# Performance work log

Hardware: AMD Instinct MI355X
Metric: run time of the kernel (lower is better)

## Reference

```python
import jax, jax.numpy as jnp
import numpy as np

N_NODES = 100000
N_GRAPHS = 128

def _graph_conv(x, W, b, s, d, n_nodes):
    """DGL GraphConv with norm='both': D_dst^{-1/2} A D_src^{-1/2} X W + b."""
    ones = jnp.ones(s.shape[0], x.dtype)
    deg_out = jax.ops.segment_sum(ones, s, num_segments=n_nodes)  # src out-degree
    deg_in = jax.ops.segment_sum(ones, d, num_segments=n_nodes)   # dst in-degree
    norm_src = jnp.where(deg_out > 0, 1.0 / jnp.sqrt(jnp.maximum(deg_out, 1.0)), 0.0)
    norm_dst = jnp.where(deg_in > 0, 1.0 / jnp.sqrt(jnp.maximum(deg_in, 1.0)), 0.0)
    h = x * norm_src[:, None]                    # [N, F]
    agg = jax.ops.segment_sum(h[s], d, num_segments=n_nodes)  # SpMM gather-scatter
    rst = (agg @ W) * norm_dst[:, None] + b
    return rst

def _hetero_layer(x, Ws, bs, src, dst, n_nodes):
    # HeteroGraphConv aggregate='sum' over relations (fixed small set -> loop ok)
    out = jnp.zeros((n_nodes, Ws.shape[-1]), x.dtype)
    for r in range(Ws.shape[0]):
        out = out + _graph_conv(x, Ws[r], bs[r], src[r], dst[r], n_nodes)
    return out

def setup_inputs() -> dict:
    key = jax.random.key(0)
    ks = jax.random.split(key, 8)
    feat = jax.random.normal(ks[0], (N_NODES, 256), dtype=jnp.float32)
    src = jax.random.randint(ks[1], (3, 400000), 0, N_NODES)
    dst = jax.random.randint(ks[2], (3, 400000), 0, N_NODES)
    graph_ids = jnp.sort(jax.random.randint(ks[3], (N_NODES,), 0, N_GRAPHS))
    W1 = jax.random.normal(ks[4], (3, 256, 256), dtype=jnp.float32) * 0.06
    b1 = jnp.zeros((3, 256), dtype=jnp.float32)
    W2 = jax.random.normal(ks[5], (3, 256, 256), dtype=jnp.float32) * 0.06
    b2 = jnp.zeros((3, 256), dtype=jnp.float32)
    return {"feat": feat, "src": src, "dst": dst, "graph_ids": graph_ids,
            "W1": W1, "b1": b1, "W2": W2, "b2": b2}

def reference(feat, src, dst, graph_ids, W1, b1, W2, b2):
    n_nodes = feat.shape[0]
    h = _hetero_layer(feat, W1, b1, src, dst, n_nodes)
    h = jax.nn.relu(h)
    h = _hetero_layer(h, W2, b2, src, dst, n_nodes)
    # AvgPooling over batched graphs
    sums = jax.ops.segment_sum(h, graph_ids, num_segments=N_GRAPHS)
    counts = jax.ops.segment_sum(jnp.ones(n_nodes, h.dtype), graph_ids, num_segments=N_GRAPHS)
    return sums / jnp.maximum(counts, 1.0)[:, None]
```

## Files before the change

kernel.cpp:

```cpp
#include <hip/hip_runtime.h>
#include <stdint.h>

#define NN 100000
#define NE 400000
#define NR 3
#define NF 256
#define NK 768
#define NG 128
#define SCAN_NB ((NN + 1023) / 1024)

typedef __attribute__((ext_vector_type(4))) unsigned short ushortx4;
typedef __attribute__((ext_vector_type(8))) unsigned short ushortx8;
typedef __attribute__((ext_vector_type(8))) short short8;
typedef __attribute__((ext_vector_type(4))) float floatx4;

static __device__ __forceinline__ unsigned short f2bfu(float f) {
  union { float f; uint32_t u; } c; c.f = f;
  uint32_t x = c.u;
  uint32_t r = (x + 0x7fffu + ((x >> 16) & 1u)) >> 16;
  return (unsigned short)r;
}
static __device__ __forceinline__ float bfu2f(unsigned short u) {
  union { uint32_t u; float f; } c; c.u = ((uint32_t)u) << 16;
  return c.f;
}

static __device__ __forceinline__ void gload16(const void* g, void* l) {
  __builtin_amdgcn_global_load_lds(
      (const __attribute__((address_space(1))) uint32_t*)g,
      (__attribute__((address_space(3))) uint32_t*)l, 16, 0, 0);
}


__global__ __launch_bounds__(256) void degree_kernel(
    const int* __restrict__ src, const int* __restrict__ dst,
    int* __restrict__ deg_out, int* __restrict__ deg_in) {
  int t = blockIdx.x * 256 + threadIdx.x;
  int r = blockIdx.y;
  if (t < NE) {
    atomicAdd(&deg_out[r * NN + src[r * NE + t]], 1);
    atomicAdd(&deg_in[r * NN + dst[r * NE + t]], 1);
  }
}

__global__ __launch_bounds__(128) void gcount_kernel(
    const int* __restrict__ gid, int* __restrict__ gcount) {
  int g = threadIdx.x;
  int lo = 0, hi = NN;
  while (lo < hi) { int mid = (lo + hi) >> 1; if (gid[mid] < g) lo = mid + 1; else hi = mid; }
  int a = lo;
  lo = 0; hi = NN;
  while (lo < hi) { int mid = (lo + hi) >> 1; if (gid[mid] < g + 1) lo = mid + 1; else hi = mid; }
  gcount[g] = lo - a;
}

__global__ __launch_bounds__(256) void norm_kernel(
    const int* __restrict__ deg_out, const int* __restrict__ deg_in,
    float* __restrict__ n_src, float* __restrict__ n_dst) {
  int t = blockIdx.x * 256 + threadIdx.x;
  if (t < NR * NN) {
    int dof = deg_out[t], din = deg_in[t];
    n_src[t] = dof > 0 ? rsqrtf((float)dof) : 0.f;
    n_dst[t] = din > 0 ? rsqrtf((float)din) : 0.f;
  }
}


__global__ __launch_bounds__(256) void scan_phaseA(
    const int* __restrict__ deg_in, int* __restrict__ blocksum) {
  int r = blockIdx.y, b = blockIdx.x, tid = threadIdx.x;
  const int* deg = deg_in + (size_t)r * NN;
  int base = b * 1024 + tid * 4;
  int s = 0;
#pragma unroll
  for (int i = 0; i < 4; ++i) { int idx = base + i; if (idx < NN) s += deg[idx]; }
  __shared__ int red[256];
  red[tid] = s; __syncthreads();
  for (int off = 128; off > 0; off >>= 1) {
    if (tid < off) red[tid] += red[tid + off];
    __syncthreads();
  }
  if (tid == 0) blocksum[r * SCAN_NB + b] = red[0];
}

__global__ __launch_bounds__(128) void scan_phaseB(
    int* __restrict__ blocksum, int* __restrict__ rowptr) {
  int r = blockIdx.x, tid = threadIdx.x;
  int* bs = blocksum + r * SCAN_NB;
  __shared__ int buf[128];
  int v = (tid < SCAN_NB) ? bs[tid] : 0;
  buf[tid] = v; __syncthreads();
  for (int off = 1; off < 128; off <<= 1) {
    int t = (tid >= off) ? buf[tid - off] : 0;
    __syncthreads();
    buf[tid] += t;
    __syncthreads();
  }
  if (tid < SCAN_NB) bs[tid] = buf[tid] - v;
  if (tid == 127) rowptr[(size_t)r * (NN + 1) + NN] = buf[127];
}

__global__ __launch_bounds__(256) void scan_phaseC(
    const int* __restrict__ deg_in, const int* __restrict__ blocksum,
    int* __restrict__ rowptr) {
  int r = blockIdx.y, b = blockIdx.x, tid = threadIdx.x;
  const int* deg = deg_in + (size_t)r * NN;
  int* rp = rowptr + (size_t)r * (NN + 1);
  int base = b * 1024 + tid * 4;
  int v[4]; int s = 0;
#pragma unroll
  for (int i = 0; i < 4; ++i) { int idx = base + i; v[i] = (idx < NN) ? deg[idx] : 0; s += v[i]; }
  __shared__ int buf[256];
  buf[tid] = s; __syncthreads();
  for (int off = 1; off < 256; off <<= 1) {
    int t = (tid >= off) ? buf[tid - off] : 0;
    __syncthreads();
    buf[tid] += t;
    __syncthreads();
  }
  int excl = buf[tid] - s + blocksum[r * SCAN_NB + b];
#pragma unroll
  for (int i = 0; i < 4; ++i) {
    int idx = base + i;
    if (idx < NN) rp[idx] = excl;
    excl += v[i];
  }
}

__global__ __launch_bounds__(256) void scatter_kernel(
    const int* __restrict__ src, const int* __restrict__ dst,
    const int* __restrict__ rowptr, int* __restrict__ cursor,
    const float* __restrict__ n_src,
    int2* __restrict__ csr_e) {
  int t = blockIdx.x * 256 + threadIdx.x;
  int r = blockIdx.y;
  if (t < NE) {
    int s = src[r * NE + t], v = dst[r * NE + t];
    int pos = atomicAdd(&cursor[r * NN + v], 1);
    int idx = r * NE + rowptr[(size_t)r * (NN + 1) + v] + pos;
    csr_e[idx] = make_int2(s, __float_as_int(n_src[r * NN + s]));
  }
}


__global__ __launch_bounds__(256) void prep_w_kernel(
    const float* __restrict__ W1, const float* __restrict__ W2,
    unsigned short* __restrict__ wt1, unsigned short* __restrict__ wt2) {
  int t = blockIdx.x * 256 + threadIdx.x;
  int lay = t / (NR * NF * NF);
  int rem = t % (NR * NF * NF);
  int r = rem / (NF * NF);
  int k = (rem / NF) % NF;
  int n = rem % NF;
  const float* W = lay ? W2 : W1;
  unsigned short* wt = lay ? wt2 : wt1;
  wt[(size_t)n * NK + r * NF + k] = f2bfu(W[((size_t)r * NF + k) * NF + n]);
}

__global__ __launch_bounds__(256) void prep_bias_kernel(
    const float* __restrict__ b1, const float* __restrict__ b2,
    float* __restrict__ bs1, float* __restrict__ bs2) {
  int t = blockIdx.x * 256 + threadIdx.x;
  if (t < 2 * NF) {
    int lay = t / NF, n = t % NF;
    const float* b = lay ? b2 : b1;
    float* bs = lay ? bs2 : bs1;
    bs[n] = b[n] + b[NF + n] + b[2 * NF + n];
  }
}

__global__ __launch_bounds__(256) void cast_kernel(
    const float* __restrict__ in, unsigned short* __restrict__ out, int n4) {
  int t = blockIdx.x * 256 + threadIdx.x;
  if (t < n4) {
    floatx4 v = *(const floatx4*)&in[(size_t)t * 4];
    ushortx4 o;
    o.x = f2bfu(v.x); o.y = f2bfu(v.y); o.z = f2bfu(v.z); o.w = f2bfu(v.w);
    *(ushortx4*)&out[(size_t)t * 4] = o;
  }
}


__global__ __launch_bounds__(256) void spmm_kernel(
    const unsigned short* __restrict__ x,
    const int* __restrict__ rowptr, const int2* __restrict__ csr_e,
    const float* __restrict__ n_dst,
    unsigned short* __restrict__ agg) {
  int wid = threadIdx.x >> 6, l = threadIdx.x & 63;
  int r = blockIdx.y;
  int v = blockIdx.x * 4 + wid;
  if (v >= NN) return;
  int e0 = rowptr[(size_t)r * (NN + 1) + v];
  int e1 = rowptr[(size_t)r * (NN + 1) + v + 1];
  const int2* ce = csr_e + (size_t)r * NE;
  const int half = l >> 5;
  const int c8 = (l & 31) * 8;

  float a[8];
#pragma unroll
  for (int j = 0; j < 8; ++j) a[j] = 0.f;

  int e = e0;
  for (; e + 4 <= e1; e += 4) {
    int2 p0 = ce[e + half];
    int2 p1 = ce[e + 2 + half];
    float w0 = __int_as_float(p0.y), w1 = __int_as_float(p1.y);
    ushortx8 x0 = *(const ushortx8*)&x[(size_t)p0.x * NF + c8];
    ushortx8 x1 = *(const ushortx8*)&x[(size_t)p1.x * NF + c8];
#pragma unroll
    for (int j = 0; j < 8; ++j) a[j] += w0 * bfu2f(x0[j]) + w1 * bfu2f(x1[j]);
  }
  for (; e < e1; e += 2) {
    int idx = e + half;
    bool ok = idx < e1;
    int2 p = ok ? ce[idx] : make_int2(0, 0);
    float w = ok ? __int_as_float(p.y) : 0.f;
    ushortx8 xv = *(const ushortx8*)&x[(size_t)p.x * NF + c8];
#pragma unroll
    for (int j = 0; j < 8; ++j) a[j] += w * bfu2f(xv[j]);
  }

#pragma unroll
  for (int j = 0; j < 8; ++j) a[j] += __shfl_xor(a[j], 32);

  if (l < 32) {
    float nd = n_dst[r * NN + v];
    ushortx8 o;
#pragma unroll
    for (int j = 0; j < 8; ++j) o[j] = f2bfu(a[j] * nd);
    *(ushortx8*)&agg[(size_t)v * NK + r * NF + c8] = o;
  }
}


__global__ __launch_bounds__(256, 2) void gemm_kernel(
    const unsigned short* __restrict__ A,
    const unsigned short* __restrict__ Bt,
    const float* __restrict__ bias,
    unsigned short* __restrict__ C,
    int M, int relu) {
  __shared__ unsigned short ldsA[128 * 32];
  __shared__ unsigned short ldsB[256 * 32];
  const int tid = threadIdx.x;
  const int l = tid & 63, wid = tid >> 6;
  const int row0 = blockIdx.x * 128;
  const int c0 = wid * 64;

  floatx4 acc[8][4];
#pragma unroll
  for (int i = 0; i < 8; ++i)
#pragma unroll
    for (int j = 0; j < 4; ++j)
#pragma unroll
      for (int q = 0; q < 4; ++q) acc[i][j][q] = 0.f;

  const int fr = l & 15, fk = (l >> 4) * 8;

  for (int kt = 0; kt < NK / 32; ++kt) {
    const int k0 = kt * 32;
    {
      int u = wid * 64 + l;
      int arow = row0 + (u >> 2);
      if (arow >= M) arow = M - 1;
      gload16(A + (size_t)arow * NK + k0 + (u & 3) * 8, &ldsA[u * 8]);
      u += 256;
      arow = row0 + (u >> 2);
      if (arow >= M) arow = M - 1;
      gload16(A + (size_t)arow * NK + k0 + (u & 3) * 8, &ldsA[u * 8]);
    }
#pragma unroll
    for (int p = 0; p < 4; ++p) {
      int u = p * 256 + wid * 64 + l;
      int col = u >> 2;
      gload16(Bt + (size_t)col * NK + k0 + (u & 3) * 8, &ldsB[u * 8]);
    }
    asm volatile("s_waitcnt vmcnt(0)" ::: "memory");
    __syncthreads();

    short8 af[8], bf[4];
#pragma unroll
    for (int m = 0; m < 8; ++m)
      af[m] = *(const short8*)&ldsA[(m * 16 + fr) * 32 + fk];
#pragma unroll
    for (int n = 0; n < 4; ++n)
      bf[n] = *(const short8*)&ldsB[(c0 + n * 16 + fr) * 32 + fk];
#pragma unroll
    for (int m = 0; m < 8; ++m)
#pragma unroll
      for (int n = 0; n < 4; ++n)
        acc[m][n] = __builtin_amdgcn_mfma_f32_16x16x32_bf16(af[m], bf[n], acc[m][n], 0, 0, 0);
    __syncthreads();
  }

  const int fq = l >> 4;
#pragma unroll
  for (int m = 0; m < 8; ++m) {
#pragma unroll
    for (int n = 0; n < 4; ++n) {
      int col = c0 + n * 16 + fr;
      float bv = bias[col];
#pragma unroll
      for (int q = 0; q < 4; ++q) {
        int row = row0 + m * 16 + fq * 4 + q;
        if (row < M) {
          float vv = acc[m][n][q] + bv;
          if (relu) vv = fmaxf(vv, 0.f);
          C[(size_t)row * NF + col] = f2bfu(vv);
        }
      }
    }
  }
}


__global__ __launch_bounds__(256) void pool_kernel(
    const unsigned short* __restrict__ h2, const int* __restrict__ gid,
    float* __restrict__ poolsum) {
  int c = threadIdx.x;
  int v0 = blockIdx.x * 256;
  int vend = min(v0 + 256, NN);
  float acc = 0.f;
  int curg = -1;
  for (int v = v0; v < vend; ++v) {
    int g = gid[v];
    if (g != curg) {
      if (curg >= 0) atomicAdd(&poolsum[curg * NF + c], acc);
      curg = g; acc = 0.f;
    }
    acc += bfu2f(h2[(size_t)v * NF + c]);
  }
  if (curg >= 0) atomicAdd(&poolsum[curg * NF + c], acc);
}

__global__ __launch_bounds__(256) void final_kernel(
    const float* __restrict__ poolsum, const int* __restrict__ gcount,
    float* __restrict__ out) {
  int g = blockIdx.x, c = threadIdx.x;
  out[g * NF + c] = poolsum[g * NF + c] / fmaxf((float)gcount[g], 1.f);
}


extern "C" void kernel_launch(void* const* d_in, const int* in_sizes, int n_in,
                              void* d_out, int out_size, void* d_ws, size_t ws_size,
                              hipStream_t stream) {
  const float* feat = (const float*)d_in[0];
  const int* src = (const int*)d_in[1];
  const int* dst = (const int*)d_in[2];
  const int* gid = (const int*)d_in[3];
  const float* W1 = (const float*)d_in[4];
  const float* b1 = (const float*)d_in[5];
  const float* W2 = (const float*)d_in[6];
  const float* b2 = (const float*)d_in[7];
  float* out = (float*)d_out;

  char* ws = (char*)d_ws;
  size_t off = 0;
  auto alloc = [&](size_t bytes) -> void* {
    void* p = ws + off;
    off = (off + bytes + 255) & ~(size_t)255;
    return p;
  };

  int* deg_out = (int*)alloc((size_t)NR * NN * 4);
  int* deg_in  = (int*)alloc((size_t)NR * NN * 4);
  int* cursor  = (int*)alloc((size_t)NR * NN * 4);
  float* poolsum = (float*)alloc((size_t)NG * NF * 4);
  size_t zero_bytes = off;

  int* gcount  = (int*)alloc((size_t)NG * 4);
  int* blocksum = (int*)alloc((size_t)NR * SCAN_NB * 4);
  float* n_src = (float*)alloc((size_t)NR * NN * 4);
  float* n_dst = (float*)alloc((size_t)NR * NN * 4);
  int* rowptr  = (int*)alloc((size_t)NR * (NN + 1) * 4);
  int2* csr_e  = (int2*)alloc((size_t)NR * NE * 8);
  unsigned short* wt1 = (unsigned short*)alloc((size_t)NF * NK * 2);
  unsigned short* wt2 = (unsigned short*)alloc((size_t)NF * NK * 2);
  float* bs1 = (float*)alloc(NF * 4);
  float* bs2 = (float*)alloc(NF * 4);
  unsigned short* featbf = (unsigned short*)alloc((size_t)NN * NF * 2);
  unsigned short* h1 = (unsigned short*)alloc((size_t)NN * NF * 2);
  unsigned short* h2 = (unsigned short*)alloc((size_t)NN * NF * 2);
  unsigned short* agg = (unsigned short*)alloc((size_t)NN * NK * 2);
  (void)ws_size; (void)in_sizes; (void)n_in; (void)out_size;

  hipMemsetAsync(d_ws, 0, zero_bytes, stream);

  dim3 eg((NE + 255) / 256, NR);
  degree_kernel<<<eg, 256, 0, stream>>>(src, dst, deg_out, deg_in);
  gcount_kernel<<<1, 128, 0, stream>>>(gid, gcount);
  norm_kernel<<<(NR * NN + 255) / 256, 256, 0, stream>>>(deg_out, deg_in, n_src, n_dst);
  scan_phaseA<<<dim3(SCAN_NB, NR), 256, 0, stream>>>(deg_in, blocksum);
  scan_phaseB<<<NR, 128, 0, stream>>>(blocksum, rowptr);
  scan_phaseC<<<dim3(SCAN_NB, NR), 256, 0, stream>>>(deg_in, blocksum, rowptr);
  scatter_kernel<<<eg, 256, 0, stream>>>(src, dst, rowptr, cursor, n_src, csr_e);

  prep_w_kernel<<<(2 * NR * NF * NF) / 256, 256, 0, stream>>>(W1, W2, wt1, wt2);
  prep_bias_kernel<<<2, 256, 0, stream>>>(b1, b2, bs1, bs2);
  cast_kernel<<<(NN * NF / 4 + 255) / 256, 256, 0, stream>>>(feat, featbf, NN * NF / 4);

  dim3 sg((NN + 3) / 4, NR);
  spmm_kernel<<<sg, 256, 0, stream>>>(featbf, rowptr, csr_e, n_dst, agg);
  gemm_kernel<<<(NN + 127) / 128, 256, 0, stream>>>(agg, wt1, bs1, h1, NN, 1);
  spmm_kernel<<<sg, 256, 0, stream>>>(h1, rowptr, csr_e, n_dst, agg);
  gemm_kernel<<<(NN + 127) / 128, 256, 0, stream>>>(agg, wt2, bs2, h2, NN, 0);
  pool_kernel<<<(NN + 255) / 256, 256, 0, stream>>>(h2, gid, poolsum);
  final_kernel<<<NG, 256, 0, stream>>>(poolsum, gcount, out);
}
```

Before: 718.4 us.

## Process all three relations per wavefront in SpMM and seed scatter cursors from rowptr

```diff
diff --git a/kernel.cpp b/kernel.cpp
--- a/kernel.cpp
+++ b/kernel.cpp
@@ -129,16 +129,14 @@
 
 __global__ __launch_bounds__(256) void scatter_kernel(
     const int* __restrict__ src, const int* __restrict__ dst,
-    const int* __restrict__ rowptr, int* __restrict__ cursor,
-    const float* __restrict__ n_src,
+    int* __restrict__ cursor, const float* __restrict__ n_src,
     int2* __restrict__ csr_e) {
   int t = blockIdx.x * 256 + threadIdx.x;
   int r = blockIdx.y;
   if (t < NE) {
     int s = src[r * NE + t], v = dst[r * NE + t];
-    int pos = atomicAdd(&cursor[r * NN + v], 1);
-    int idx = r * NE + rowptr[(size_t)r * (NN + 1) + v] + pos;
-    csr_e[idx] = make_int2(s, __float_as_int(n_src[r * NN + s]));
+    int pos = atomicAdd(&cursor[r * (NN + 1) + v], 1);
+    csr_e[(size_t)r * NE + pos] = make_int2(s, __float_as_int(n_src[r * NN + s]));
   }
 }
 
@@ -187,48 +185,71 @@
     const float* __restrict__ n_dst,
     unsigned short* __restrict__ agg) {
   int wid = threadIdx.x >> 6, l = threadIdx.x & 63;
-  int r = blockIdx.y;
   int v = blockIdx.x * 4 + wid;
   if (v >= NN) return;
-  int e0 = rowptr[(size_t)r * (NN + 1) + v];
-  int e1 = rowptr[(size_t)r * (NN + 1) + v + 1];
-  const int2* ce = csr_e + (size_t)r * NE;
   const int half = l >> 5;
   const int c8 = (l & 31) * 8;
 
-  float a[8];
-#pragma unroll
-  for (int j = 0; j < 8; ++j) a[j] = 0.f;
-
-  int e = e0;
-  for (; e + 4 <= e1; e += 4) {
-    int2 p0 = ce[e + half];
-    int2 p1 = ce[e + 2 + half];
-    float w0 = __int_as_float(p0.y), w1 = __int_as_float(p1.y);
-    ushortx8 x0 = *(const ushortx8*)&x[(size_t)p0.x * NF + c8];
-    ushortx8 x1 = *(const ushortx8*)&x[(size_t)p1.x * NF + c8];
-#pragma unroll
-    for (int j = 0; j < 8; ++j) a[j] += w0 * bfu2f(x0[j]) + w1 * bfu2f(x1[j]);
-  }
-  for (; e < e1; e += 2) {
-    int idx = e + half;
-    bool ok = idx < e1;
-    int2 p = ok ? ce[idx] : make_int2(0, 0);
-    float w = ok ? __int_as_float(p.y) : 0.f;
-    ushortx8 xv = *(const ushortx8*)&x[(size_t)p.x * NF + c8];
-#pragma unroll
-    for (int j = 0; j < 8; ++j) a[j] += w * bfu2f(xv[j]);
-  }
-
-#pragma unroll
-  for (int j = 0; j < 8; ++j) a[j] += __shfl_xor(a[j], 32);
+  int ea = rowptr[v],                e1a = rowptr[v + 1];
+  int eb = rowptr[(NN + 1) + v],     e1b = rowptr[(NN + 1) + v + 1];
+  int ec = rowptr[2 * (NN + 1) + v], e1c = rowptr[2 * (NN + 1) + v + 1];
+  const int2* cea = csr_e;
+  const int2* ceb = csr_e + (size_t)NE;
+  const int2* cec = csr_e + (size_t)2 * NE;
+
+  float a[NR][8];
+#pragma unroll
+  for (int r = 0; r < NR; ++r)
+#pragma unroll
+    for (int j = 0; j < 8; ++j) a[r][j] = 0.f;
+
+  while (ea < e1a || eb < e1b || ec < e1c) {
+    if (ea < e1a) {
+      if (ea + half < e1a) {
+        int2 p = cea[ea + half];
+        float w = __int_as_float(p.y);
+        ushortx8 xv = *(const ushortx8*)&x[(size_t)p.x * NF + c8];
+#pragma unroll
+        for (int j = 0; j < 8; ++j) a[0][j] += w * bfu2f(xv[j]);
+      }
+      ea += 2;
+    }
+    if (eb < e1b) {
+      if (eb + half < e1b) {
+        int2 p = ceb[eb + half];
+        float w = __int_as_float(p.y);
+        ushortx8 xv = *(const ushortx8*)&x[(size_t)p.x * NF + c8];
+#pragma unroll
+        for (int j = 0; j < 8; ++j) a[1][j] += w * bfu2f(xv[j]);
+      }
+      eb += 2;
+    }
+    if (ec < e1c) {
+      if (ec + half < e1c) {
+        int2 p = cec[ec + half];
+        float w = __int_as_float(p.y);
+        ushortx8 xv = *(const ushortx8*)&x[(size_t)p.x * NF + c8];
+#pragma unroll
+        for (int j = 0; j < 8; ++j) a[2][j] += w * bfu2f(xv[j]);
+      }
+      ec += 2;
+    }
+  }
+
+#pragma unroll
+  for (int r = 0; r < NR; ++r)
+#pragma unroll
+    for (int j = 0; j < 8; ++j) a[r][j] += __shfl_xor(a[r][j], 32);
 
   if (l < 32) {
-    float nd = n_dst[r * NN + v];
-    ushortx8 o;
-#pragma unroll
-    for (int j = 0; j < 8; ++j) o[j] = f2bfu(a[j] * nd);
-    *(ushortx8*)&agg[(size_t)v * NK + r * NF + c8] = o;
+#pragma unroll
+    for (int r = 0; r < NR; ++r) {
+      float nd = n_dst[r * NN + v];
+      ushortx8 o;
+#pragma unroll
+      for (int j = 0; j < 8; ++j) o[j] = f2bfu(a[r][j] * nd);
+      *(ushortx8*)&agg[(size_t)v * NK + r * NF + c8] = o;
+    }
   }
 }
 
@@ -363,10 +384,10 @@
 
   int* deg_out = (int*)alloc((size_t)NR * NN * 4);
   int* deg_in  = (int*)alloc((size_t)NR * NN * 4);
-  int* cursor  = (int*)alloc((size_t)NR * NN * 4);
   float* poolsum = (float*)alloc((size_t)NG * NF * 4);
   size_t zero_bytes = off;
 
+  int* cursor  = (int*)alloc((size_t)NR * (NN + 1) * 4);
   int* gcount  = (int*)alloc((size_t)NG * 4);
   int* blocksum = (int*)alloc((size_t)NR * SCAN_NB * 4);
   float* n_src = (float*)alloc((size_t)NR * NN * 4);
@@ -392,16 +413,17 @@
   scan_phaseA<<<dim3(SCAN_NB, NR), 256, 0, stream>>>(deg_in, blocksum);
   scan_phaseB<<<NR, 128, 0, stream>>>(blocksum, rowptr);
   scan_phaseC<<<dim3(SCAN_NB, NR), 256, 0, stream>>>(deg_in, blocksum, rowptr);
-  scatter_kernel<<<eg, 256, 0, stream>>>(src, dst, rowptr, cursor, n_src, csr_e);
+  hipMemcpyAsync(cursor, rowptr, (size_t)NR * (NN + 1) * 4,
+                 hipMemcpyDeviceToDevice, stream);
+  scatter_kernel<<<eg, 256, 0, stream>>>(src, dst, cursor, n_src, csr_e);
 
   prep_w_kernel<<<(2 * NR * NF * NF) / 256, 256, 0, stream>>>(W1, W2, wt1, wt2);
   prep_bias_kernel<<<2, 256, 0, stream>>>(b1, b2, bs1, bs2);
   cast_kernel<<<(NN * NF / 4 + 255) / 256, 256, 0, stream>>>(feat, featbf, NN * NF / 4);
 
-  dim3 sg((NN + 3) / 4, NR);
-  spmm_kernel<<<sg, 256, 0, stream>>>(featbf, rowptr, csr_e, n_dst, agg);
+  spmm_kernel<<<(NN + 3) / 4, 256, 0, stream>>>(featbf, rowptr, csr_e, n_dst, agg);
   gemm_kernel<<<(NN + 127) / 128, 256, 0, stream>>>(agg, wt1, bs1, h1, NN, 1);
-  spmm_kernel<<<sg, 256, 0, stream>>>(h1, rowptr, csr_e, n_dst, agg);
+  spmm_kernel<<<(NN + 3) / 4, 256, 0, stream>>>(h1, rowptr, csr_e, n_dst, agg);
   gemm_kernel<<<(NN + 127) / 128, 256, 0, stream>>>(agg, wt2, bs2, h2, NN, 0);
   pool_kernel<<<(NN + 255) / 256, 256, 0, stream>>>(h2, gid, poolsum);
   final_kernel<<<NG, 256, 0, stream>>>(poolsum, gcount, out);
```

Result: no change. 713.2 us (-0.7%).
